# Kernel tuning notes

Hardware: AMD Instinct MI355X
Metric: run time of the kernel (lower is better)

The kernel has to match this reference:

```python
import jax, jax.numpy as jnp
import numpy as np

N = 100000   # nodes
E = 1600000  # edges (before self-loops)
DIN, DH, DL = 128, 128, 64


def setup_inputs() -> dict:
    key = jax.random.key(0)
    ks = jax.random.split(key, 6)
    feat = jax.random.normal(ks[0], (N, DIN), dtype=jnp.float32)
    src = jax.random.randint(ks[1], (E,), 0, N)
    dst = jax.random.randint(ks[2], (E,), 0, N)

    def glorot(k, i, o):
        return jax.random.normal(k, (i, o), dtype=jnp.float32) * (1.0 / np.sqrt(i))

    return dict(
        feat=feat, src=src, dst=dst,
        W1=glorot(ks[3], DIN, DH), b1=jnp.zeros((DH,), jnp.float32),
        W2=glorot(ks[4], DH, DH), b2=jnp.zeros((DH,), jnp.float32),
        W3=glorot(ks[5], DH, DL), b3=jnp.zeros((DL,), jnp.float32),
    )


def _graph_conv(feat, src, dst, out_isqrt, in_isqrt, W, b):
    # DGL GraphConv, norm='both': scale src by d_out^{-1/2}, sum messages
    # into dst, scale by d_in^{-1/2}, then dense transform.
    h = feat * out_isqrt[:, None]                                   # [N, F]
    agg = jax.ops.segment_sum(h[src], dst, num_segments=N)          # [N, F]
    agg = agg * in_isqrt[:, None]
    return agg @ W + b


def reference(feat, src, dst, W1, b1, W2, b2, W3, b3):
    # dgl.add_self_loop: append (i, i) for every node
    loops = jnp.arange(N, dtype=src.dtype)
    s = jnp.concatenate([src, loops])
    d = jnp.concatenate([dst, loops])

    ones = jnp.ones(s.shape[0], dtype=feat.dtype)
    deg_out = jax.ops.segment_sum(ones, s, num_segments=N)
    deg_in = jax.ops.segment_sum(ones, d, num_segments=N)
    out_isqrt = jax.lax.rsqrt(jnp.maximum(deg_out, 1.0))
    in_isqrt = jax.lax.rsqrt(jnp.maximum(deg_in, 1.0))

    h = jax.nn.relu(_graph_conv(feat, s, d, out_isqrt, in_isqrt, W1, b1))
    h = jax.nn.relu(_graph_conv(h, s, d, out_isqrt, in_isqrt, W2, b2))
    return _graph_conv(h, s, d, out_isqrt, in_isqrt, W3, b3)
```

## Files before the change

kernel.cpp:

```cpp
#include <hip/hip_runtime.h>
#include <hip/hip_fp16.h>

#define NN 100000
#define NE 1600000
#define KDIM 128

#define BSH 8
#define NBKT ((NN + 255) >> BSH)
#define BCAP 6144
#define CHUNK 4096
#define CPAD 16

#define SRC_MASK 0x1FFFFu

typedef _Float16 half8 __attribute__((ext_vector_type(8)));
typedef float f32x4 __attribute__((ext_vector_type(4)));

template <int NOUT>
__device__ inline void packW_body(const float* __restrict__ W, _Float16* __restrict__ Wp,
                                  int blk) {
    constexpr int NT = NOUT / 16;
    int idx = blk * 256 + threadIdx.x;
    if (idx >= 128 * NOUT) return;
    int j = idx & 7;
    int l = (idx >> 3) & 63;
    int rest = idx >> 9;
    int nt = rest % NT;
    int kt = rest / NT;
    int k = kt * 32 + ((l >> 4) & 3) * 8 + j;
    int n = nt * 16 + (l & 15);
    Wp[idx] = (_Float16)W[(size_t)k * NOUT + n];
}

__global__ __launch_bounds__(256) void k_prep(const float* __restrict__ W1,
                                              const float* __restrict__ W2,
                                              const float* __restrict__ W3,
                                              _Float16* __restrict__ Wp1,
                                              _Float16* __restrict__ Wp2,
                                              _Float16* __restrict__ Wp3,
                                              unsigned* __restrict__ cursor_d,
                                              unsigned* __restrict__ cursor_s) {
    int b = blockIdx.x;
    if (b < 64) packW_body<128>(W1, Wp1, b);
    else if (b < 128) packW_body<128>(W2, Wp2, b - 64);
    else if (b < 160) packW_body<64>(W3, Wp3, b - 128);
    else {
        for (int k = threadIdx.x; k < NBKT; k += 256) {
            cursor_d[(size_t)k * CPAD] = (unsigned)k * BCAP;
            cursor_s[(size_t)k * CPAD] = (unsigned)k * BCAP;
        }
    }
}

__global__ __launch_bounds__(256) void k_cvt(const float* __restrict__ f,
                                             __half* __restrict__ o) {
    int i = blockIdx.x * 256 + threadIdx.x;
    if (i < NN * KDIM / 8) {
        const float4* f4 = (const float4*)f + 2 * (size_t)i;
        float4 a = f4[0], b = f4[1];
        __half2 h0 = __floats2half2_rn(a.x, a.y);
        __half2 h1 = __floats2half2_rn(a.z, a.w);
        __half2 h2 = __floats2half2_rn(b.x, b.y);
        __half2 h3 = __floats2half2_rn(b.z, b.w);
        __half2 hh[4] = {h0, h1, h2, h3};
        *((uint4*)o + i) = *(uint4*)hh;
    }
}

__global__ __launch_bounds__(512) void k_part2(const int* __restrict__ src,
                                               const int* __restrict__ dst,
                                               unsigned* __restrict__ cursor_d,
                                               unsigned* __restrict__ cursor_s,
                                               unsigned* __restrict__ part_d,
                                               unsigned char* __restrict__ part_s) {
    __shared__ unsigned histd[NBKT];
    __shared__ unsigned hists[NBKT];
    __shared__ unsigned lofsd[NBKT], lofss[NBKT];
    __shared__ unsigned gbased[NBKT], gbases[NBKT];
    __shared__ unsigned sbuf[512];
    __shared__ unsigned staged[CHUNK];
    __shared__ unsigned short stagebd[CHUNK];
    __shared__ unsigned char stages[CHUNK];
    __shared__ unsigned short stagebs[CHUNK];

    const int e0 = blockIdx.x * CHUNK;
    const int lim = min(CHUNK, NE - e0);
    const int t = threadIdx.x;

    for (int k = t; k < NBKT; k += 512) {
        histd[k] = 0u;
        hists[k] = 0u;
    }
    __syncthreads();

    unsigned es[CHUNK / 512], ed[CHUNK / 512];
    int nmine = 0;
#pragma unroll
    for (int i = 0; i < CHUNK / 512; ++i) {
        int r = t + i * 512;
        if (r < lim) {
            es[i] = (unsigned)src[e0 + r];
            ed[i] = (unsigned)dst[e0 + r];
            atomicAdd(&histd[ed[i] >> BSH], 1u);
            atomicAdd(&hists[es[i] >> BSH], 1u);
            nmine = i + 1;
        }
    }
    __syncthreads();

    unsigned vd = (t < NBKT) ? histd[t] : 0u;
    unsigned vs = (t < NBKT) ? hists[t] : 0u;
    unsigned v = (vd << 16) | vs;
    sbuf[t] = v;
    __syncthreads();
    for (int off = 1; off < 512; off <<= 1) {
        unsigned x = sbuf[t];
        if (t >= off) x += sbuf[t - off];
        __syncthreads();
        sbuf[t] = x;
        __syncthreads();
    }
    if (t < NBKT) {
        unsigned ld = (sbuf[t] >> 16) - vd;
        unsigned ls = (sbuf[t] & 0xFFFFu) - vs;
        lofsd[t] = ld;
        lofss[t] = ls;
        gbased[t] = (vd ? atomicAdd(&cursor_d[(size_t)t * CPAD], vd) : 0u) - ld;
        gbases[t] = (vs ? atomicAdd(&cursor_s[(size_t)t * CPAD], vs) : 0u) - ls;
        histd[t] = 0u;
        hists[t] = 0u;
    }
    __syncthreads();

#pragma unroll
    for (int i = 0; i < CHUNK / 512; ++i) {
        if (i < nmine) {
            unsigned kd = ed[i] >> BSH;
            unsigned pd = lofsd[kd] + atomicAdd(&histd[kd], 1u);
            staged[pd] = es[i] | ((ed[i] & 255u) << 17);
            stagebd[pd] = (unsigned short)kd;
            unsigned ks = es[i] >> BSH;
            unsigned ps = lofss[ks] + atomicAdd(&hists[ks], 1u);
            stages[ps] = (unsigned char)(es[i] & 255u);
            stagebs[ps] = (unsigned short)ks;
        }
    }
    __syncthreads();

    for (int j = t; j < lim; j += 512) {
        unsigned k = stagebd[j];
        unsigned gaddr = gbased[k] + (unsigned)j;
        if (gaddr - k * BCAP < BCAP)
            part_d[gaddr] = staged[j];
        unsigned k2 = stagebs[j];
        unsigned gaddr2 = gbases[k2] + (unsigned)j;
        if (gaddr2 - k2 * BCAP < BCAP)
            part_s[gaddr2] = stages[j];
    }
}

__global__ __launch_bounds__(256) void k_build(const unsigned* __restrict__ cursor_d,
                                               const unsigned* __restrict__ cursor_s,
                                               const unsigned* __restrict__ part_d,
                                               const unsigned char* __restrict__ part_s,
                                               unsigned* __restrict__ cnt_in,
                                               float* __restrict__ oi,
                                               float* __restrict__ ii,
                                               unsigned* __restrict__ row_start,
                                               unsigned* __restrict__ csr) {
    __shared__ unsigned c[256];
    __shared__ unsigned c2[256];
    __shared__ unsigned s[256];
    __shared__ unsigned red[256];
    __shared__ unsigned cur[256];
    __shared__ unsigned stage[BCAP];
    const int b = blockIdx.x;
    const int t = threadIdx.x;

    unsigned ps = 0;
    for (int k = t; k < b; k += 256)
        ps += min(cursor_d[(size_t)k * CPAD] - (unsigned)k * BCAP, (unsigned)BCAP);
    red[t] = ps;
    c[t] = 0u;
    c2[t] = 0u;
    __syncthreads();
    for (int off = 128; off > 0; off >>= 1) {
        if (t < off) red[t] += red[t + off];
        __syncthreads();
    }
    const unsigned prefix = red[0];

    unsigned cntd = min(cursor_d[(size_t)b * CPAD] - (unsigned)b * BCAP, (unsigned)BCAP);
    unsigned cnts = min(cursor_s[(size_t)b * CPAD] - (unsigned)b * BCAP, (unsigned)BCAP);
    const unsigned* ppd = part_d + (size_t)b * BCAP;
    const unsigned char* pps = part_s + (size_t)b * BCAP;
    for (unsigned j = t; j < cntd; j += 256)
        atomicAdd(&c[(ppd[j] >> 17) & 255u], 1u);
    for (unsigned j = t; j < cnts; j += 256)
        atomicAdd(&c2[pps[j]], 1u);
    __syncthreads();

    unsigned v = c[t];
    s[t] = v;
    __syncthreads();
    for (int off = 1; off < 256; off <<= 1) {
        unsigned x = s[t];
        if (t >= off) x += s[t - off];
        __syncthreads();
        s[t] = x;
        __syncthreads();
    }
    int node = (b << BSH) + t;
    if (node < NN) {
        cnt_in[node] = v;
        ii[node] = rsqrtf((float)(v + 1u));
        oi[node] = rsqrtf((float)(c2[t] + 1u));
        row_start[node] = prefix + s[t] - v;
    }
    cur[t] = s[t] - v;
    __syncthreads();

    for (unsigned j = t; j < cntd; j += 256) {
        unsigned e = ppd[j];
        unsigned p = atomicAdd(&cur[(e >> 17) & 255u], 1u);
        stage[p] = e & SRC_MASK;
    }
    __syncthreads();
    for (unsigned j = t; j < cntd; j += 256)
        csr[prefix + j] = stage[j];
}

template <bool SCALE_SRC>
__global__ __launch_bounds__(256) void k_aggemm(const __half* __restrict__ h,
                                                const float* __restrict__ oi,
                                                const float* __restrict__ ii,
                                                const unsigned* __restrict__ row_start,
                                                const unsigned* __restrict__ cnt_in,
                                                const unsigned* __restrict__ csr,
                                                const _Float16* __restrict__ Wp,
                                                const float* __restrict__ bias,
                                                _Float16* __restrict__ Y16) {
    constexpr int NT = 8;
    __shared__ _Float16 As[4][16][136];
    const int w = threadIdx.x >> 6;
    const int lane = threadIdx.x & 63;
    const int r0 = blockIdx.x * 64 + w * 16;
    const __half2* hv = (const __half2*)h;

    for (int i = 0; i < 16; ++i) {
        int wid = r0 + i;
        if (wid >= NN) break;
        float2 acc;
        {
            float2 vv = __half22float2(hv[(size_t)wid * 64 + lane]);
            float sc = SCALE_SRC ? oi[wid] : 1.f;
            acc.x = vv.x * sc;
            acc.y = vv.y * sc;
        }
        unsigned rs = row_start[wid];
        unsigned nk = cnt_in[wid];
        for (unsigned base = 0; base < nk; base += 64) {
            unsigned m = min(64u, nk - base);
            unsigned myidx = ((unsigned)lane < m) ? csr[rs + base + lane] : 0u;
            unsigned k = 0;
            for (; k + 16 <= m; k += 16) {
                unsigned sidx[16];
                float sc[16];
                __half2 vv[16];
#pragma unroll
                for (int q = 0; q < 16; ++q) {
                    sidx[q] = (unsigned)__builtin_amdgcn_readlane((int)myidx, (int)(k + q));
                    vv[q] = hv[(size_t)sidx[q] * 64 + lane];
                    if (SCALE_SRC) sc[q] = oi[sidx[q]];
                }
#pragma unroll
                for (int q = 0; q < 16; ++q) {
                    float2 f = __half22float2(vv[q]);
                    if (SCALE_SRC) {
                        acc.x = fmaf(f.x, sc[q], acc.x);
                        acc.y = fmaf(f.y, sc[q], acc.y);
                    } else {
                        acc.x += f.x;
                        acc.y += f.y;
                    }
                }
            }
            if (k < m) {
                unsigned sidx[16];
                float sc[16];
                __half2 vv[16];
#pragma unroll
                for (int q = 0; q < 16; ++q) {
                    sidx[q] = (unsigned)__builtin_amdgcn_readlane((int)myidx, (int)(k + q));
                    vv[q] = hv[(size_t)sidx[q] * 64 + lane];
                    float wq = SCALE_SRC ? oi[sidx[q]] : 1.f;
                    sc[q] = (k + q < m) ? wq : 0.f;
                }
#pragma unroll
                for (int q = 0; q < 16; ++q) {
                    float2 f = __half22float2(vv[q]);
                    acc.x = fmaf(f.x, sc[q], acc.x);
                    acc.y = fmaf(f.y, sc[q], acc.y);
                }
            }
        }
        float si = ii[wid];
        *(__half2*)&As[w][i][lane * 2] = __floats2half2_rn(acc.x * si, acc.y * si);
    }

    const half8* Bp = (const half8*)Wp + lane;
    f32x4 acc[NT];
#pragma unroll
    for (int n = 0; n < NT; ++n) acc[n] = {0.f, 0.f, 0.f, 0.f};
    const int fr = lane & 15;
    const int fg = lane >> 4;
#pragma unroll
    for (int kt = 0; kt < 4; ++kt) {
        half8 a = *(const half8*)&As[w][fr][kt * 32 + fg * 8];
#pragma unroll
        for (int n = 0; n < NT; ++n) {
            half8 b = Bp[(kt * NT + n) * 64];
            acc[n] = __builtin_amdgcn_mfma_f32_16x16x32_f16(a, b, acc[n], 0, 0, 0);
        }
    }

    const int col = lane & 15;
    const int rbase = r0 + (lane >> 4) * 4;
#pragma unroll
    for (int j = 0; j < 4; ++j) {
        int row = rbase + j;
        if (row >= NN) continue;
        float os = oi[row];
#pragma unroll
        for (int n = 0; n < NT; ++n) {
            float vv = acc[n][j] + bias[n * 16 + col];
            vv = fmaxf(vv, 0.f);
            Y16[(size_t)row * 128 + n * 16 + col] = (_Float16)(vv * os);
        }
    }
}

__global__ __launch_bounds__(256) void k_agg64h(const __half* __restrict__ t,
                                                const float* __restrict__ ii,
                                                const float* __restrict__ bias,
                                                const unsigned* __restrict__ row_start,
                                                const unsigned* __restrict__ cnt_in,
                                                const unsigned* __restrict__ csr,
                                                float* __restrict__ out) {
    int wid = (int)((blockIdx.x * 256u + threadIdx.x) >> 6);
    int lane = threadIdx.x & 63;
    if (wid >= NN) return;
    float acc = __half2float(t[(size_t)wid * 64 + lane]);
    unsigned rs = row_start[wid];
    unsigned nk = cnt_in[wid];
    for (unsigned base = 0; base < nk; base += 64) {
        unsigned m = min(64u, nk - base);
        unsigned myidx = ((unsigned)lane < m) ? csr[rs + base + lane] : 0u;
        unsigned k = 0;
        for (; k + 16 <= m; k += 16) {
            unsigned s[16];
            __half v[16];
#pragma unroll
            for (int i = 0; i < 16; ++i) {
                s[i] = (unsigned)__builtin_amdgcn_readlane((int)myidx, (int)(k + i));
                v[i] = t[(size_t)s[i] * 64 + lane];
            }
#pragma unroll
            for (int i = 0; i < 16; ++i) acc += __half2float(v[i]);
        }
        if (k < m) {
            unsigned s[16];
            float sc[16];
            __half v[16];
#pragma unroll
            for (int i = 0; i < 16; ++i) {
                s[i] = (unsigned)__builtin_amdgcn_readlane((int)myidx, (int)(k + i));
                v[i] = t[(size_t)s[i] * 64 + lane];
                sc[i] = (k + i < m) ? 1.f : 0.f;
            }
#pragma unroll
            for (int i = 0; i < 16; ++i) acc = fmaf(__half2float(v[i]), sc[i], acc);
        }
    }
    out[(size_t)wid * 64 + lane] = acc * ii[wid] + bias[lane];
}

template <int NOUT>
__global__ __launch_bounds__(256) void k_gemmf(const _Float16* __restrict__ A,
                                               const _Float16* __restrict__ Wp,
                                               _Float16* __restrict__ Y16) {
    constexpr int NT = NOUT / 16;
    const int w = threadIdx.x >> 6;
    const int l = threadIdx.x & 63;
    const int r0 = blockIdx.x * 128 + w * 32;
    int arow0 = r0 + (l & 15);
    int arow1 = arow0 + 16;
    if (arow0 >= NN) arow0 = NN - 1;
    if (arow1 >= NN) arow1 = NN - 1;
    const half8* Ap0 = (const half8*)(A + (size_t)arow0 * 128) + (l >> 4);
    const half8* Ap1 = (const half8*)(A + (size_t)arow1 * 128) + (l >> 4);
    const half8* Bp = (const half8*)Wp + l;

    f32x4 acc0[NT], acc1[NT];
#pragma unroll
    for (int n = 0; n < NT; ++n) {
        acc0[n] = {0.f, 0.f, 0.f, 0.f};
        acc1[n] = {0.f, 0.f, 0.f, 0.f};
    }

#pragma unroll
    for (int kt = 0; kt < 4; ++kt) {
        half8 a0 = Ap0[kt * 4];
        half8 a1 = Ap1[kt * 4];
#pragma unroll
        for (int n = 0; n < NT; ++n) {
            half8 b = Bp[(kt * NT + n) * 64];
            acc0[n] = __builtin_amdgcn_mfma_f32_16x16x32_f16(a0, b, acc0[n], 0, 0, 0);
            acc1[n] = __builtin_amdgcn_mfma_f32_16x16x32_f16(a1, b, acc1[n], 0, 0, 0);
        }
    }

    const int col = l & 15;
#pragma unroll
    for (int half = 0; half < 2; ++half) {
        const int rbase = r0 + half * 16 + (l >> 4) * 4;
        f32x4* acc = half ? acc1 : acc0;
#pragma unroll
        for (int j = 0; j < 4; ++j) {
            int row = rbase + j;
            if (row >= NN) continue;
#pragma unroll
            for (int n = 0; n < NT; ++n)
                Y16[(size_t)row * NOUT + n * 16 + col] = (_Float16)acc[n][j];
        }
    }
}

extern "C" void kernel_launch(void* const* d_in, const int* in_sizes, int n_in,
                              void* d_out, int out_size, void* d_ws, size_t ws_size,
                              hipStream_t stream) {
    const float* feat = (const float*)d_in[0];
    const int* src = (const int*)d_in[1];
    const int* dst = (const int*)d_in[2];
    const float* W1 = (const float*)d_in[3];
    const float* b1 = (const float*)d_in[4];
    const float* W2 = (const float*)d_in[5];
    const float* b2 = (const float*)d_in[6];
    const float* W3 = (const float*)d_in[7];
    const float* b3 = (const float*)d_in[8];
    float* out = (float*)d_out;

    char* p = (char*)d_ws;
    auto take = [&](size_t bytes) {
        char* q = p;
        p += (bytes + 255) & ~(size_t)255;
        return q;
    };
    unsigned* cnt_in = (unsigned*)take((size_t)NN * 4);
    float* oi = (float*)take((size_t)NN * 4);
    float* ii = (float*)take((size_t)NN * 4);
    unsigned* row_start = (unsigned*)take((size_t)NN * 4);
    unsigned* cursor_d = (unsigned*)take((size_t)NBKT * CPAD * 4);
    unsigned* cursor_s = (unsigned*)take((size_t)NBKT * CPAD * 4);
    unsigned* csr = (unsigned*)take((size_t)NE * 4);
    unsigned char* part_s = (unsigned char*)take((size_t)NBKT * BCAP);
    __half* feat16 = (__half*)take((size_t)NN * KDIM * 2);
    __half* H16 = (__half*)take((size_t)NN * KDIM * 2);
    __half* G16 = (__half*)take((size_t)NN * KDIM * 2);
    _Float16* Wp1 = (_Float16*)take((size_t)128 * 128 * 2);
    _Float16* Wp2 = (_Float16*)take((size_t)128 * 128 * 2);
    _Float16* Wp3 = (_Float16*)take((size_t)128 * 64 * 2);
    char* regionB = take((size_t)NN * 64 * 2 > (size_t)NBKT * BCAP * 4
                             ? (size_t)NN * 64 * 2
                             : (size_t)NBKT * BCAP * 4);
    unsigned* part_d = (unsigned*)regionB;
    __half* T16 = (__half*)regionB;

    k_prep<<<161, 256, 0, stream>>>(W1, W2, W3, Wp1, Wp2, Wp3, cursor_d, cursor_s);
    k_cvt<<<(NN * KDIM / 8 + 255) / 256, 256, 0, stream>>>(feat, feat16);
    k_part2<<<(NE + CHUNK - 1) / CHUNK, 512, 0, stream>>>(src, dst, cursor_d, cursor_s,
                                                          part_d, part_s);
    k_build<<<NBKT, 256, 0, stream>>>(cursor_d, cursor_s, part_d, part_s, cnt_in, oi, ii,
                                      row_start, csr);

    const int FUSED_BLOCKS = (NN + 63) / 64;
    const int AGG_BLOCKS = (NN + 3) / 4;
    const int GEMM_BLOCKS = (NN + 127) / 128;

    k_aggemm<true><<<FUSED_BLOCKS, 256, 0, stream>>>(feat16, oi, ii, row_start, cnt_in,
                                                     csr, Wp1, b1, (_Float16*)H16);
    k_aggemm<false><<<FUSED_BLOCKS, 256, 0, stream>>>(H16, oi, ii, row_start, cnt_in,
                                                      csr, Wp2, b2, (_Float16*)G16);
    k_gemmf<64><<<GEMM_BLOCKS, 256, 0, stream>>>((const _Float16*)G16, Wp3, (_Float16*)T16);
    k_agg64h<<<AGG_BLOCKS, 256, 0, stream>>>(T16, ii, b3, row_start, cnt_in, csr, out);
}
```

Measured before the change: 327.8 us.

## Split aggregate+GEMM kernels, fuse layer-2 and layer-3 GEMMs, merge cvt into prep

Replaces the fused aggregate-then-MFMA kernels with a separate one-wave-per-node gather kernel followed by standalone GEMM kernels. Layer 2's GEMM (with bias, ReLU and out-degree scaling) is fused with layer 3's 128->64 GEMM through shared memory, which removes one full write and read of the hidden matrix. The feature fp16 conversion is folded into the prep launch to drop one kernel launch. The split adds an extra round trip of the aggregated 128-wide matrix through global memory for each layer, in exchange for better occupancy in the gather and a simpler GEMM phase.

```diff
diff --git a/kernel.cpp b/kernel.cpp
--- a/kernel.cpp
+++ b/kernel.cpp
@@ -12,6 +12,8 @@
 #define CPAD 16
 
 #define SRC_MASK 0x1FFFFu
+
+#define CVT_BLOCKS (NN * KDIM / 8 / 256)
 
 typedef _Float16 half8 __attribute__((ext_vector_type(8)));
 typedef float f32x4 __attribute__((ext_vector_type(4)));
@@ -39,31 +41,30 @@
                                               _Float16* __restrict__ Wp2,
                                               _Float16* __restrict__ Wp3,
                                               unsigned* __restrict__ cursor_d,
-                                              unsigned* __restrict__ cursor_s) {
+                                              unsigned* __restrict__ cursor_s,
+                                              const float* __restrict__ f,
+                                              __half* __restrict__ o) {
     int b = blockIdx.x;
     if (b < 64) packW_body<128>(W1, Wp1, b);
     else if (b < 128) packW_body<128>(W2, Wp2, b - 64);
     else if (b < 160) packW_body<64>(W3, Wp3, b - 128);
-    else {
+    else if (b == 160) {
         for (int k = threadIdx.x; k < NBKT; k += 256) {
             cursor_d[(size_t)k * CPAD] = (unsigned)k * BCAP;
             cursor_s[(size_t)k * CPAD] = (unsigned)k * BCAP;
         }
-    }
-}
-
-__global__ __launch_bounds__(256) void k_cvt(const float* __restrict__ f,
-                                             __half* __restrict__ o) {
-    int i = blockIdx.x * 256 + threadIdx.x;
-    if (i < NN * KDIM / 8) {
-        const float4* f4 = (const float4*)f + 2 * (size_t)i;
-        float4 a = f4[0], b = f4[1];
-        __half2 h0 = __floats2half2_rn(a.x, a.y);
-        __half2 h1 = __floats2half2_rn(a.z, a.w);
-        __half2 h2 = __floats2half2_rn(b.x, b.y);
-        __half2 h3 = __floats2half2_rn(b.z, b.w);
-        __half2 hh[4] = {h0, h1, h2, h3};
-        *((uint4*)o + i) = *(uint4*)hh;
+    } else {
+        int i = (b - 161) * 256 + threadIdx.x;
+        if (i < NN * KDIM / 8) {
+            const float4* f4 = (const float4*)f + 2 * (size_t)i;
+            float4 a = f4[0], bb = f4[1];
+            __half2 h0 = __floats2half2_rn(a.x, a.y);
+            __half2 h1 = __floats2half2_rn(a.z, a.w);
+            __half2 h2 = __floats2half2_rn(bb.x, bb.y);
+            __half2 h3 = __floats2half2_rn(bb.z, bb.w);
+            __half2 hh[4] = {h0, h1, h2, h3};
+            *((uint4*)o + i) = *(uint4*)hh;
+        }
     }
 }
 
@@ -231,113 +232,73 @@
 }
 
 template <bool SCALE_SRC>
-__global__ __launch_bounds__(256) void k_aggemm(const __half* __restrict__ h,
-                                                const float* __restrict__ oi,
-                                                const float* __restrict__ ii,
-                                                const unsigned* __restrict__ row_start,
-                                                const unsigned* __restrict__ cnt_in,
-                                                const unsigned* __restrict__ csr,
-                                                const _Float16* __restrict__ Wp,
-                                                const float* __restrict__ bias,
-                                                _Float16* __restrict__ Y16) {
-    constexpr int NT = 8;
-    __shared__ _Float16 As[4][16][136];
-    const int w = threadIdx.x >> 6;
-    const int lane = threadIdx.x & 63;
-    const int r0 = blockIdx.x * 64 + w * 16;
+__global__ __launch_bounds__(256) void k_agg128h(const __half* __restrict__ h,
+                                                 const float* __restrict__ oi,
+                                                 const float* __restrict__ ii,
+                                                 const unsigned* __restrict__ row_start,
+                                                 const unsigned* __restrict__ cnt_in,
+                                                 const unsigned* __restrict__ csr,
+                                                 __half* __restrict__ out) {
+    int wid = (int)((blockIdx.x * 256u + threadIdx.x) >> 6);
+    int lane = threadIdx.x & 63;
+    if (wid >= NN) return;
     const __half2* hv = (const __half2*)h;
-
-    for (int i = 0; i < 16; ++i) {
-        int wid = r0 + i;
-        if (wid >= NN) break;
-        float2 acc;
-        {
-            float2 vv = __half22float2(hv[(size_t)wid * 64 + lane]);
-            float sc = SCALE_SRC ? oi[wid] : 1.f;
-            acc.x = vv.x * sc;
-            acc.y = vv.y * sc;
-        }
-        unsigned rs = row_start[wid];
-        unsigned nk = cnt_in[wid];
-        for (unsigned base = 0; base < nk; base += 64) {
-            unsigned m = min(64u, nk - base);
-            unsigned myidx = ((unsigned)lane < m) ? csr[rs + base + lane] : 0u;
-            unsigned k = 0;
-            for (; k + 16 <= m; k += 16) {
-                unsigned sidx[16];
-                float sc[16];
-                __half2 vv[16];
-#pragma unroll
-                for (int q = 0; q < 16; ++q) {
-                    sidx[q] = (unsigned)__builtin_amdgcn_readlane((int)myidx, (int)(k + q));
-                    vv[q] = hv[(size_t)sidx[q] * 64 + lane];
-                    if (SCALE_SRC) sc[q] = oi[sidx[q]];
+    float2 acc;
+    {
+        float2 v = __half22float2(hv[(size_t)wid * 64 + lane]);
+        float sc = SCALE_SRC ? oi[wid] : 1.f;
+        acc.x = v.x * sc;
+        acc.y = v.y * sc;
+    }
+    unsigned rs = row_start[wid];
+    unsigned nk = cnt_in[wid];
+    for (unsigned base = 0; base < nk; base += 64) {
+        unsigned m = min(64u, nk - base);
+        unsigned myidx = ((unsigned)lane < m) ? csr[rs + base + lane] : 0u;
+        unsigned k = 0;
+        for (; k + 16 <= m; k += 16) {
+            unsigned s[16];
+            float sc[16];
+            __half2 v[16];
+#pragma unroll
+            for (int i = 0; i < 16; ++i) {
+                s[i] = (unsigned)__builtin_amdgcn_readlane((int)myidx, (int)(k + i));
+                v[i] = hv[(size_t)s[i] * 64 + lane];
+                if (SCALE_SRC) sc[i] = oi[s[i]];
+            }
+#pragma unroll
+            for (int i = 0; i < 16; ++i) {
+                float2 f = __half22float2(v[i]);
+                if (SCALE_SRC) {
+                    acc.x = fmaf(f.x, sc[i], acc.x);
+                    acc.y = fmaf(f.y, sc[i], acc.y);
+                } else {
+                    acc.x += f.x;
+                    acc.y += f.y;
                 }
-#pragma unroll
-                for (int q = 0; q < 16; ++q) {
-                    float2 f = __half22float2(vv[q]);
-                    if (SCALE_SRC) {
-                        acc.x = fmaf(f.x, sc[q], acc.x);
-                        acc.y = fmaf(f.y, sc[q], acc.y);
-                    } else {
-                        acc.x += f.x;
-                        acc.y += f.y;
-                    }
-                }
-            }
-            if (k < m) {
-                unsigned sidx[16];
-                float sc[16];
-                __half2 vv[16];
-#pragma unroll
-                for (int q = 0; q < 16; ++q) {
-                    sidx[q] = (unsigned)__builtin_amdgcn_readlane((int)myidx, (int)(k + q));
-                    vv[q] = hv[(size_t)sidx[q] * 64 + lane];
-                    float wq = SCALE_SRC ? oi[sidx[q]] : 1.f;
-                    sc[q] = (k + q < m) ? wq : 0.f;
-                }
-#pragma unroll
-                for (int q = 0; q < 16; ++q) {
-                    float2 f = __half22float2(vv[q]);
-                    acc.x = fmaf(f.x, sc[q], acc.x);
-                    acc.y = fmaf(f.y, sc[q], acc.y);
-                }
-            }
-        }
-        float si = ii[wid];
-        *(__half2*)&As[w][i][lane * 2] = __floats2half2_rn(acc.x * si, acc.y * si);
-    }
-
-    const half8* Bp = (const half8*)Wp + lane;
-    f32x4 acc[NT];
-#pragma unroll
-    for (int n = 0; n < NT; ++n) acc[n] = {0.f, 0.f, 0.f, 0.f};
-    const int fr = lane & 15;
-    const int fg = lane >> 4;
-#pragma unroll
-    for (int kt = 0; kt < 4; ++kt) {
-        half8 a = *(const half8*)&As[w][fr][kt * 32 + fg * 8];
-#pragma unroll
-        for (int n = 0; n < NT; ++n) {
-            half8 b = Bp[(kt * NT + n) * 64];
-            acc[n] = __builtin_amdgcn_mfma_f32_16x16x32_f16(a, b, acc[n], 0, 0, 0);
-        }
-    }
-
-    const int col = lane & 15;
-    const int rbase = r0 + (lane >> 4) * 4;
-#pragma unroll
-    for (int j = 0; j < 4; ++j) {
-        int row = rbase + j;
-        if (row >= NN) continue;
-        float os = oi[row];
-#pragma unroll
-        for (int n = 0; n < NT; ++n) {
-            float vv = acc[n][j] + bias[n * 16 + col];
-            vv = fmaxf(vv, 0.f);
-            Y16[(size_t)row * 128 + n * 16 + col] = (_Float16)(vv * os);
-        }
-    }
+            }
+        }
+        if (k < m) {
+            unsigned s[16];
+            float sc[16];
+            __half2 v[16];
+#pragma unroll
+            for (int i = 0; i < 16; ++i) {
+                s[i] = (unsigned)__builtin_amdgcn_readlane((int)myidx, (int)(k + i));
+                v[i] = hv[(size_t)s[i] * 64 + lane];
+                float w = SCALE_SRC ? oi[s[i]] : 1.f;
+                sc[i] = (k + i < m) ? w : 0.f;
+            }
+#pragma unroll
+            for (int i = 0; i < 16; ++i) {
+                float2 f = __half22float2(v[i]);
+                acc.x = fmaf(f.x, sc[i], acc.x);
+                acc.y = fmaf(f.y, sc[i], acc.y);
+            }
+        }
+    }
+    float si = ii[wid];
+    ((__half2*)out)[(size_t)wid * 64 + lane] = __floats2half2_rn(acc.x * si, acc.y * si);
 }
 
 __global__ __launch_bounds__(256) void k_agg64h(const __half* __restrict__ t,
@@ -385,11 +346,12 @@
     out[(size_t)wid * 64 + lane] = acc * ii[wid] + bias[lane];
 }
 
-template <int NOUT>
-__global__ __launch_bounds__(256) void k_gemmf(const _Float16* __restrict__ A,
+__global__ __launch_bounds__(256) void k_gemm1(const _Float16* __restrict__ A,
                                                const _Float16* __restrict__ Wp,
+                                               const float* __restrict__ bias,
+                                               const float* __restrict__ oscale,
                                                _Float16* __restrict__ Y16) {
-    constexpr int NT = NOUT / 16;
+    constexpr int NT = 8;
     const int w = threadIdx.x >> 6;
     const int l = threadIdx.x & 63;
     const int r0 = blockIdx.x * 128 + w * 32;
@@ -407,7 +369,6 @@
         acc0[n] = {0.f, 0.f, 0.f, 0.f};
         acc1[n] = {0.f, 0.f, 0.f, 0.f};
     }
-
 #pragma unroll
     for (int kt = 0; kt < 4; ++kt) {
         half8 a0 = Ap0[kt * 4];
@@ -419,7 +380,6 @@
             acc1[n] = __builtin_amdgcn_mfma_f32_16x16x32_f16(a1, b, acc1[n], 0, 0, 0);
         }
     }
-
     const int col = l & 15;
 #pragma unroll
     for (int half = 0; half < 2; ++half) {
@@ -429,10 +389,80 @@
         for (int j = 0; j < 4; ++j) {
             int row = rbase + j;
             if (row >= NN) continue;
-#pragma unroll
-            for (int n = 0; n < NT; ++n)
-                Y16[(size_t)row * NOUT + n * 16 + col] = (_Float16)acc[n][j];
-        }
+            float os = oscale[row];
+#pragma unroll
+            for (int n = 0; n < NT; ++n) {
+                float v = fmaxf(acc[n][j] + bias[n * 16 + col], 0.f);
+                Y16[(size_t)row * 128 + n * 16 + col] = (_Float16)(v * os);
+            }
+        }
+    }
+}
+
+__global__ __launch_bounds__(256) void k_gemm23(const _Float16* __restrict__ A,
+                                                const _Float16* __restrict__ Wp2,
+                                                const _Float16* __restrict__ Wp3,
+                                                const float* __restrict__ bias,
+                                                const float* __restrict__ oscale,
+                                                _Float16* __restrict__ T16) {
+    constexpr int NT = 8;
+    __shared__ _Float16 As[4][16][136];
+    const int w = threadIdx.x >> 6;
+    const int l = threadIdx.x & 63;
+    const int r0 = blockIdx.x * 64 + w * 16;
+    int arow = r0 + (l & 15);
+    if (arow >= NN) arow = NN - 1;
+    const half8* Ap = (const half8*)(A + (size_t)arow * 128) + (l >> 4);
+    const half8* Bp2 = (const half8*)Wp2 + l;
+    const half8* Bp3 = (const half8*)Wp3 + l;
+
+    f32x4 acc[NT];
+#pragma unroll
+    for (int n = 0; n < NT; ++n) acc[n] = {0.f, 0.f, 0.f, 0.f};
+#pragma unroll
+    for (int kt = 0; kt < 4; ++kt) {
+        half8 a = Ap[kt * 4];
+#pragma unroll
+        for (int n = 0; n < NT; ++n) {
+            half8 b = Bp2[(kt * NT + n) * 64];
+            acc[n] = __builtin_amdgcn_mfma_f32_16x16x32_f16(a, b, acc[n], 0, 0, 0);
+        }
+    }
+
+    const int col = l & 15;
+    const int rloc = (l >> 4) * 4;
+#pragma unroll
+    for (int j = 0; j < 4; ++j) {
+        int row = r0 + rloc + j;
+        float os = (row < NN) ? oscale[row] : 0.f;
+#pragma unroll
+        for (int n = 0; n < NT; ++n) {
+            float v = fmaxf(acc[n][j] + bias[n * 16 + col], 0.f);
+            As[w][rloc + j][n * 16 + col] = (_Float16)(v * os);
+        }
+    }
+
+    f32x4 acc2[4];
+#pragma unroll
+    for (int n = 0; n < 4; ++n) acc2[n] = {0.f, 0.f, 0.f, 0.f};
+    const int fr = l & 15;
+    const int fg = l >> 4;
+#pragma unroll
+    for (int kt = 0; kt < 4; ++kt) {
+        half8 a = *(const half8*)&As[w][fr][kt * 32 + fg * 8];
+#pragma unroll
+        for (int n = 0; n < 4; ++n) {
+            half8 b = Bp3[(kt * 4 + n) * 64];
+            acc2[n] = __builtin_amdgcn_mfma_f32_16x16x32_f16(a, b, acc2[n], 0, 0, 0);
+        }
+    }
+#pragma unroll
+    for (int j = 0; j < 4; ++j) {
+        int row = r0 + rloc + j;
+        if (row >= NN) continue;
+#pragma unroll
+        for (int n = 0; n < 4; ++n)
+            T16[(size_t)row * 64 + n * 16 + col] = (_Float16)acc2[n][j];
     }
 }
 
@@ -476,21 +506,22 @@
     unsigned* part_d = (unsigned*)regionB;
     __half* T16 = (__half*)regionB;
 
-    k_prep<<<161, 256, 0, stream>>>(W1, W2, W3, Wp1, Wp2, Wp3, cursor_d, cursor_s);
-    k_cvt<<<(NN * KDIM / 8 + 255) / 256, 256, 0, stream>>>(feat, feat16);
+    k_prep<<<161 + CVT_BLOCKS, 256, 0, stream>>>(W1, W2, W3, Wp1, Wp2, Wp3, cursor_d,
+                                                 cursor_s, feat, feat16);
     k_part2<<<(NE + CHUNK - 1) / CHUNK, 512, 0, stream>>>(src, dst, cursor_d, cursor_s,
                                                           part_d, part_s);
     k_build<<<NBKT, 256, 0, stream>>>(cursor_d, cursor_s, part_d, part_s, cnt_in, oi, ii,
                                       row_start, csr);
 
-    const int FUSED_BLOCKS = (NN + 63) / 64;
     const int AGG_BLOCKS = (NN + 3) / 4;
-    const int GEMM_BLOCKS = (NN + 127) / 128;
-
-    k_aggemm<true><<<FUSED_BLOCKS, 256, 0, stream>>>(feat16, oi, ii, row_start, cnt_in,
-                                                     csr, Wp1, b1, (_Float16*)H16);
-    k_aggemm<false><<<FUSED_BLOCKS, 256, 0, stream>>>(H16, oi, ii, row_start, cnt_in,
-                                                      csr, Wp2, b2, (_Float16*)G16);
-    k_gemmf<64><<<GEMM_BLOCKS, 256, 0, stream>>>((const _Float16*)G16, Wp3, (_Float16*)T16);
+    const int GEMM1_BLOCKS = (NN + 127) / 128;
+    const int GEMM23_BLOCKS = (NN + 63) / 64;
+
+    k_agg128h<true><<<AGG_BLOCKS, 256, 0, stream>>>(feat16, oi, ii, row_start, cnt_in, csr, G16);
+    k_gemm1<<<GEMM1_BLOCKS, 256, 0, stream>>>((const _Float16*)G16, Wp1, b1, oi,
+                                              (_Float16*)H16);
+    k_agg128h<false><<<AGG_BLOCKS, 256, 0, stream>>>(H16, oi, ii, row_start, cnt_in, csr, G16);
+    k_gemm23<<<GEMM23_BLOCKS, 256, 0, stream>>>((const _Float16*)G16, Wp2, Wp3, b2, oi,
+                                                (_Float16*)T16);
     k_agg64h<<<AGG_BLOCKS, 256, 0, stream>>>(T16, ii, b3, row_start, cnt_in, csr, out);
 }
```

After: 271.8 us. 17.1% less time.
